# Optimization experiments

Measured on AMD Instinct MI355X. Metric: run time of the kernel, lower is better.

The kernel has to match this reference:

```python
import jax, jax.numpy as jnp
import numpy as np

B, S, D = 8, 2048, 768
NEG_SLOPE = 0.2  # PyG GATConv default LeakyReLU slope


def setup_inputs() -> dict:
    key = jax.random.key(0)
    ks = jax.random.split(key, 8)
    scale = 0.02
    return {
        "hidden_states": jax.random.normal(ks[0], (B, S, D), jnp.float32),
        "transformer_output": jax.random.normal(ks[1], (B, S, D), jnp.float32),
        "W_gat": jax.random.normal(ks[2], (D, D), jnp.float32) * scale,
        "a_src": jax.random.normal(ks[3], (D,), jnp.float32) * scale,
        "a_dst": jax.random.normal(ks[4], (D,), jnp.float32) * scale,
        "b_gat": jnp.zeros((D,), jnp.float32),
        "W_fus": jax.random.normal(ks[5], (2 * D, D), jnp.float32) * scale,
        "b_fus": jnp.zeros((D,), jnp.float32),
    }


def reference(hidden_states, transformer_output, W_gat, a_src, a_dst, b_gat, W_fus, b_fus):
    # GATConv (heads=1) over a complete graph (build_graph gives all i!=j edges,
    # PyG GATConv then adds self-loops) => dense softmax attention over all S nodes.
    xp = jnp.einsum("bsd,de->bse", hidden_states, W_gat)          # [B,S,D] transformed nodes
    alpha_src = jnp.einsum("bsd,d->bs", xp, a_src)                # score contrib of source j
    alpha_dst = jnp.einsum("bsd,d->bs", xp, a_dst)                # score contrib of target i
    # e[b,i,j] = LeakyReLU(alpha_dst[b,i] + alpha_src[b,j])
    e = jax.nn.leaky_relu(alpha_dst[:, :, None] + alpha_src[:, None, :], NEG_SLOPE)
    attn = jax.nn.softmax(e, axis=-1)                              # softmax over sources j per target i
    graph_out = jnp.einsum("bij,bjd->bid", attn, xp) + b_gat       # aggregate + bias
    fused = jnp.concatenate([transformer_output, graph_out], axis=-1)
    return jnp.einsum("bsf,fd->bsd", fused, W_fus) + b_fus
```

## Files before the change

kernel.cpp:

```cpp
#include <hip/hip_runtime.h>
#include <hip/hip_bf16.h>
#include <stdint.h>

#define B_   8
#define S_   2048
#define D_   768
#define BS_  16384
#define F_   1536

typedef __attribute__((ext_vector_type(8))) short short8;
typedef __attribute__((ext_vector_type(4))) float f32x4;
typedef __attribute__((ext_vector_type(4))) float float4v;
typedef __attribute__((ext_vector_type(4))) unsigned short ushort4v;

__device__ __forceinline__ unsigned short f2bf(float f) {
  union { float f; unsigned u; } v; v.f = f;
  unsigned r = v.u + 0x7FFFu + ((v.u >> 16) & 1u);
  return (unsigned short)(r >> 16);
}
__device__ __forceinline__ float bf2f(unsigned short h) {
  union { unsigned u; float f; } v; v.u = ((unsigned)h) << 16;
  return v.f;
}
__device__ __forceinline__ unsigned cvtpk_bf16(float lo, float hi) {
  unsigned r; asm("v_cvt_pk_bf16_f32 %0, %1, %2" : "=v"(r) : "v"(lo), "v"(hi)); return r;
}

#define GLOAD16(gp, lp) \
  __builtin_amdgcn_global_load_lds((const __attribute__((address_space(1))) void*)(gp), \
                                   (__attribute__((address_space(3))) void*)(lp), 16, 0, 0)

__global__ __launch_bounds__(256) void k_cast8(const float* __restrict__ s1,
                                               unsigned short* __restrict__ d1, int n) {
  int i = (blockIdx.x * 256 + threadIdx.x) * 8;
  if (i >= n) return;
  float4v a = *(const float4v*)(s1 + i);
  float4v b2 = *(const float4v*)(s1 + i + 4);
  union { short8 s; unsigned u[4]; } o;
  o.u[0] = cvtpk_bf16(a[0], a[1]); o.u[1] = cvtpk_bf16(a[2], a[3]);
  o.u[2] = cvtpk_bf16(b2[0], b2[1]); o.u[3] = cvtpk_bf16(b2[2], b2[3]);
  *(short8*)(d1 + i) = o.s;
}

__global__ __launch_bounds__(256) void k_transpose_cast(const float* __restrict__ src,
                                                        unsigned short* __restrict__ dst,
                                                        int R, int C) {
  __shared__ float tile[32][33];
  int bx = blockIdx.x * 32;
  int by = blockIdx.y * 32;
  int tx = threadIdx.x, ty = threadIdx.y;
#pragma unroll
  for (int k = 0; k < 32; k += 8)
    tile[ty + k][tx] = src[(size_t)(by + ty + k) * C + bx + tx];
  __syncthreads();
#pragma unroll
  for (int k = 0; k < 32; k += 8)
    dst[(size_t)(bx + ty + k) * R + by + tx] = f2bf(tile[tx][ty + k]);
}

template <int EPI>
__global__ __launch_bounds__(256, 2) void k_gemm(const unsigned short* __restrict__ A,
                                                 const unsigned short* __restrict__ A2,
                                                 const unsigned short* __restrict__ BT,
                                                 int K, int Ksplit,
                                                 float* __restrict__ outF,
                                                 const float* __restrict__ bias,
                                                 unsigned short* __restrict__ outT,
                                                 const float* __restrict__ aS,
                                                 const float* __restrict__ aD,
                                                 float* __restrict__ asO,
                                                 float* __restrict__ adO) {
  __shared__ unsigned short smem[32768];
  int lin = blockIdx.x;
  int nl  = (lin & 7) * 96 + (lin >> 3);
  int mBase = (nl / 6) * 128;
  int nBase = (nl % 6) * 128;
  int t = threadIdx.x;
  int w = t >> 6, l = t & 63;
  int lm = l & 15, lg = l >> 4;
  int wm = w >> 1, wn = w & 1;
  f32x4 acc[4][4] = {};
  const int KT = K >> 6;

  auto stage = [&](int kt, int half) {
    unsigned short* Ab = smem + half * 16384;
    unsigned short* Bb = Ab + 8192;
    const unsigned short* As = (kt < Ksplit) ? A : A2;
    int ka = (kt < Ksplit) ? kt : kt - Ksplit;
#pragma unroll
    for (int i = 0; i < 4; ++i) {
      int g = i * 256 + t;
      int r = g >> 3;
      int c = (g & 7) ^ (r & 7);
      GLOAD16(As + (size_t)(mBase + r) * 768 + ka + c * 8, (char*)Ab + i * 4096 + w * 1024);
      GLOAD16(BT + (size_t)(nBase + r) * K + kt + c * 8, (char*)Bb + i * 4096 + w * 1024);
    }
  };

  stage(0, 0);
  for (int kt = 0; kt < KT; ++kt) {
    int half = kt & 1;
    if (kt + 1 < KT) {
      stage((kt + 1) * 64, half ^ 1);
      asm volatile("s_waitcnt vmcnt(8)" ::: "memory");
    } else {
      asm volatile("s_waitcnt vmcnt(0)" ::: "memory");
    }
    __builtin_amdgcn_s_barrier();
    __builtin_amdgcn_sched_barrier(0);
    unsigned short* Ab = smem + half * 16384;
    unsigned short* Bb = Ab + 8192;
    __builtin_amdgcn_s_setprio(1);
#pragma unroll
    for (int ks = 0; ks < 2; ++ks) {
      short8 af[4], bfr[4];
#pragma unroll
      for (int mi = 0; mi < 4; ++mi) {
        int r = wm * 64 + mi * 16 + lm;
        int c = (ks * 4 + lg) ^ (r & 7);
        af[mi] = *(const short8*)(Ab + r * 64 + c * 8);
      }
#pragma unroll
      for (int ni = 0; ni < 4; ++ni) {
        int r = wn * 64 + ni * 16 + lm;
        int c = (ks * 4 + lg) ^ (r & 7);
        bfr[ni] = *(const short8*)(Bb + r * 64 + c * 8);
      }
#pragma unroll
      for (int mi = 0; mi < 4; ++mi)
#pragma unroll
        for (int ni = 0; ni < 4; ++ni)
          acc[mi][ni] = __builtin_amdgcn_mfma_f32_16x16x32_bf16(af[mi], bfr[ni], acc[mi][ni], 0, 0, 0);
    }
    __builtin_amdgcn_s_setprio(0);
    __builtin_amdgcn_sched_barrier(0);
    __builtin_amdgcn_s_barrier();
  }

  if (EPI == 0) {
#pragma unroll
    for (int mi = 0; mi < 4; ++mi) {
      int m = mBase + wm * 64 + mi * 16 + lg * 4;
#pragma unroll
      for (int ni = 0; ni < 4; ++ni) {
        int n = nBase + wn * 64 + ni * 16 + lm;
        float bv = bias[n];
#pragma unroll
        for (int r = 0; r < 4; ++r)
          outF[(size_t)(m + r) * 768 + n] = acc[mi][ni][r] + bv;
      }
    }
  } else {
#pragma unroll
    for (int mi = 0; mi < 4; ++mi) {
#pragma unroll
      for (int ni = 0; ni < 4; ++ni) {
        int col = wn * 64 + ni * 16 + lm;
#pragma unroll
        for (int r = 0; r < 4; ++r) {
          int row = wm * 64 + mi * 16 + lg * 4 + r;
          int phys = (((col >> 3) ^ (row & 7)) << 3) | (col & 7);
          smem[row * 128 + phys] = f2bf(acc[mi][ni][r]);
        }
      }
    }
    float* aLds = (float*)(smem + 16384);
    if (t < 128) {
      aLds[t] = aS[nBase + t];
      aLds[128 + t] = aD[nBase + t];
    }
    __syncthreads();
#pragma unroll
    for (int it = 0; it < 8; ++it) {
      int row = it * 16 + (t >> 4);
      int gg = t & 15;
      short8 v = *(const short8*)(&smem[row * 128 + ((gg ^ (row & 7)) << 3)]);
      *(short8*)(outT + (size_t)(mBase + row) * 768 + nBase + gg * 8) = v;
    }
    {
      int row = t >> 1, halfc = t & 1;
      float accs = 0.f, accd = 0.f;
#pragma unroll
      for (int gg = 0; gg < 8; ++gg) {
        int cq = halfc * 8 + gg;
        short8 v = *(const short8*)(&smem[row * 128 + ((cq ^ (row & 7)) << 3)]);
#pragma unroll
        for (int e = 0; e < 8; ++e) {
          float x = bf2f((unsigned short)v[e]);
          accs = fmaf(aLds[cq * 8 + e], x, accs);
          accd = fmaf(aLds[128 + cq * 8 + e], x, accd);
        }
      }
      accs += __shfl_xor(accs, 1);
      accd += __shfl_xor(accd, 1);
      if (halfc == 0) {
        atomicAdd(asO + mBase + row, accs);
        atomicAdd(adO + mBase + row, accd);
      }
    }
  }
}

__global__ __launch_bounds__(256) void k_rank(const float* __restrict__ as,
                                              float* __restrict__ ssorted, int* __restrict__ sidx,
                                              float* __restrict__ es1g, float* __restrict__ es2g,
                                              float* __restrict__ msg) {
  __shared__ float sjl[S_];
  __shared__ float red[256];
  __shared__ int rk[32][9];
  int b = blockIdx.y, t = threadIdx.x;
  float lmx = -1e30f;
#pragma unroll
  for (int q = 0; q < 2; ++q) {
    int p = (t + q * 256) * 4;
    float4v v = *(const float4v*)(as + b * S_ + p);
    *(float4v*)(sjl + p) = v;
    lmx = fmaxf(lmx, fmaxf(fmaxf(v[0], v[1]), fmaxf(v[2], v[3])));
  }
  red[t] = lmx;
  __syncthreads();
  for (int st = 128; st > 0; st >>= 1) {
    if (t < st) red[t] = fmaxf(red[t], red[t + st]);
    __syncthreads();
  }
  float Ms = red[0];
  int jl = t & 31, part = t >> 5;
  int j = blockIdx.x * 32 + jl;
  float sj = sjl[j];
  int r0 = 0, r1 = 0, r2 = 0, r3 = 0;
  int kbase = part * 256;
#pragma unroll 8
  for (int kq = 0; kq < 64; ++kq) {
    int k = kbase + kq * 4;
    float4v sk = *(const float4v*)(sjl + k);
    r0 += (sk[0] < sj) | ((sk[0] == sj) & (k < j));
    r1 += (sk[1] < sj) | ((sk[1] == sj) & (k + 1 < j));
    r2 += (sk[2] < sj) | ((sk[2] == sj) & (k + 2 < j));
    r3 += (sk[3] < sj) | ((sk[3] == sj) & (k + 3 < j));
  }
  rk[jl][part] = r0 + r1 + r2 + r3;
  __syncthreads();
  if (t < 32) {
    int rank = rk[t][0] + rk[t][1] + rk[t][2] + rk[t][3]
             + rk[t][4] + rk[t][5] + rk[t][6] + rk[t][7];
    int jj = blockIdx.x * 32 + t;
    float sv = sjl[jj];
    ssorted[b * S_ + rank] = sv;
    sidx[b * S_ + rank] = jj;
    es1g[b * S_ + rank] = __expf(sv - Ms);
    es2g[b * S_ + rank] = __expf(0.2f * (sv - Ms));
    if (blockIdx.x == 0 && t == 0) msg[b] = Ms;
  }
}

__global__ __launch_bounds__(256) void k_pscan(const float* __restrict__ es1g,
                                               const float* __restrict__ es2g,
                                               float* __restrict__ sufug,
                                               float* __restrict__ prevg) {
  __shared__ float su[256], pv[256];
  int b = blockIdx.x, t = threadIdx.x;
  float a1 = 0.f, a2 = 0.f;
#pragma unroll
  for (int r = 0; r < 8; ++r) {
    a1 += es1g[b * S_ + t * 8 + r];
    a2 += es2g[b * S_ + t * 8 + r];
  }
  su[t] = a1; pv[t] = a2;
  __syncthreads();
  for (int off = 1; off < 256; off <<= 1) {
    float vs = (t + off < 256) ? su[t + off] : 0.f;
    float vp = (t >= off) ? pv[t - off] : 0.f;
    __syncthreads();
    su[t] += vs; pv[t] += vp;
    __syncthreads();
  }
  sufug[b * 260 + t] = su[t];
  prevg[b * 260 + t] = (t > 0) ? pv[t - 1] : 0.f;
  if (t == 0) sufug[b * 260 + 256] = 0.f;
}

__global__ __launch_bounds__(192) void k_chunks(const unsigned short* __restrict__ xp,
                                                const int* __restrict__ sidx,
                                                const float* __restrict__ es1g,
                                                const float* __restrict__ es2g,
                                                float* __restrict__ SU, float* __restrict__ SV) {
  __shared__ int ridx[64];
  __shared__ float w1l[64], w2l[64];
  int b = blockIdx.y, cblk = blockIdx.x;
  int t = threadIdx.x;
  if (t < 64) {
    int r = cblk * 64 + t;
    ridx[t] = sidx[b * S_ + r];
    w1l[t] = es1g[b * S_ + r];
    w2l[t] = es2g[b * S_ + r];
  }
  __syncthreads();
  int d0 = t * 4;
  const unsigned short* xb = xp + (size_t)b * S_ * D_;
  for (int q = 0; q < 8; ++q) {
    float a1[4] = {0.f, 0.f, 0.f, 0.f}, a2[4] = {0.f, 0.f, 0.f, 0.f};
#pragma unroll
    for (int r = 0; r < 8; ++r) {
      int j = q * 8 + r;
      ushort4v xv = *(const ushort4v*)(xb + (size_t)ridx[j] * D_ + d0);
      float w1 = w1l[j], w2 = w2l[j];
#pragma unroll
      for (int e = 0; e < 4; ++e) {
        float x = bf2f(xv[e]);
        a1[e] = fmaf(w1, x, a1[e]);
        a2[e] = fmaf(w2, x, a2[e]);
      }
    }
    int c = cblk * 8 + q;
    float4v o1, o2;
    o1[0] = a1[0]; o1[1] = a1[1]; o1[2] = a1[2]; o1[3] = a1[3];
    o2[0] = a2[0]; o2[1] = a2[1]; o2[2] = a2[2]; o2[3] = a2[3];
    *(float4v*)(SU + ((size_t)b * 257 + c) * D_ + d0) = o1;
    *(float4v*)(SV + ((size_t)b * 256 + c) * D_ + d0) = o2;
  }
}

__global__ __launch_bounds__(256) void k_scan(float* __restrict__ SU, float* __restrict__ SV) {
  __shared__ float sums[8][33];
  int b = blockIdx.y;
  int dl = threadIdx.x & 31, p = threadIdx.x >> 5;
  int d = blockIdx.x * 32 + dl;
  float* u = SU + (size_t)b * 257 * D_ + d;
  float* v = SV + (size_t)b * 256 * D_ + d;
  int c0 = p * 32;
  float cu[32], cv[32];
  float su_ = 0.f, sv_ = 0.f;
#pragma unroll
  for (int q = 0; q < 32; ++q) {
    cu[q] = u[(size_t)(c0 + q) * D_];
    cv[q] = v[(size_t)(c0 + q) * D_];
    su_ += cu[q]; sv_ += cv[q];
  }
  sums[p][dl] = su_;
  __syncthreads();
  float offU = 0.f;
#pragma unroll
  for (int q = 0; q < 8; ++q) if (q > p) offU += sums[q][dl];
  __syncthreads();
  sums[p][dl] = sv_;
  __syncthreads();
  float offV = 0.f;
#pragma unroll
  for (int q = 0; q < 8; ++q) if (q < p) offV += sums[q][dl];
  float run = offU;
#pragma unroll
  for (int q = 31; q >= 0; --q) { run += cu[q]; u[(size_t)(c0 + q) * D_] = run; }
  float pr = offV;
#pragma unroll
  for (int q = 0; q < 32; ++q) { v[(size_t)(c0 + q) * D_] = pr; pr += cv[q]; }
  if (p == 0) u[(size_t)256 * D_] = 0.f;
}

__global__ __launch_bounds__(256) void k_out(const unsigned short* __restrict__ xp,
                                             const float* __restrict__ ad,
                                             const float* __restrict__ ssorted,
                                             const int* __restrict__ sidx,
                                             const float* __restrict__ es1g,
                                             const float* __restrict__ es2g,
                                             const float* __restrict__ sufug,
                                             const float* __restrict__ prevg,
                                             const float* __restrict__ msg,
                                             const float* __restrict__ SU,
                                             const float* __restrict__ SV,
                                             const float* __restrict__ b_gat,
                                             const float* __restrict__ to,
                                             unsigned short* __restrict__ to_bf,
                                             unsigned short* __restrict__ gout) {
  __shared__ float skeys[2048];
  __shared__ float G1[8], G2[8], WL[8][8];
  __shared__ int CI[8], RI[8][8];
  int bid = blockIdx.x;
  int b = bid & 7, itile = bid >> 3;
  int i0 = itile * 8;
  int t = threadIdx.x;
#pragma unroll
  for (int k2 = 0; k2 < 2; ++k2) {
    int p = (t + k2 * 256) * 4;
    *(float4v*)(skeys + p) = *(const float4v*)(ssorted + b * S_ + p);
  }
  __syncthreads();
  if (t < 8) {
    int i = i0 + t;
    float di = ad[b * S_ + i];
    float thr = -di;
    int lo = 0, hi = 2048;
#pragma unroll
    for (int st = 0; st < 11; ++st) {
      int mid = (lo + hi) >> 1;
      if (skeys[mid] <= thr) lo = mid + 1; else hi = mid;
    }
    int c = lo >> 3; if (c > 255) c = 255;
    float t1 = di + msg[b];
    float mst = fmaxf(t1, 0.2f * t1);
    float g1 = __expf(t1 - mst), g2 = __expf(0.2f * t1 - mst);
    float den = g1 * sufug[b * 260 + c + 1] + g2 * prevg[b * 260 + c];
    float wr[8]; int rid[8];
#pragma unroll
    for (int r = 0; r < 8; ++r) {
      int row = c * 8 + r;
      bool neg = (skeys[row] <= thr);
      float wv = neg ? g2 * es2g[b * S_ + row] : g1 * es1g[b * S_ + row];
      den += wv;
      wr[r] = wv;
      rid[r] = sidx[b * S_ + row];
    }
    float inv = 1.f / den;
    G1[t] = g1 * inv; G2[t] = g2 * inv; CI[t] = c;
#pragma unroll
    for (int r = 0; r < 8; ++r) { WL[t][r] = wr[r] * inv; RI[t][r] = rid[r]; }
  }
  __syncthreads();
  int w = t >> 6, lane = t & 63;
  int dbase = lane * 4;
  float4v bgv[3];
#pragma unroll
  for (int q = 0; q < 3; ++q) bgv[q] = *(const float4v*)(b_gat + dbase + q * 256);
  const unsigned short* xb = xp + (size_t)b * S_ * D_;
  const float* SUb = SU + (size_t)b * 257 * D_;
  const float* SVb = SV + (size_t)b * 256 * D_;
#pragma unroll
  for (int rep = 0; rep < 2; ++rep) {
    int ii = w + rep * 4;
    int c = CI[ii];
    float g1 = G1[ii], g2 = G2[ii];
    size_t roff = ((size_t)(b * S_ + i0 + ii)) * D_;
    float4v o[3];
#pragma unroll
    for (int q = 0; q < 3; ++q) {
      int d = dbase + q * 256;
      float4v uu = *(const float4v*)(SUb + (size_t)(c + 1) * D_ + d);
      float4v vv = *(const float4v*)(SVb + (size_t)c * D_ + d);
#pragma unroll
      for (int e = 0; e < 4; ++e) o[q][e] = fmaf(g1, uu[e], g2 * vv[e]);
    }
#pragma unroll
    for (int q = 0; q < 3; ++q) {
      int d = dbase + q * 256;
      float4v tv = *(const float4v*)(to + roff + d);
      ushort4v ow;
      ow[0] = f2bf(tv[0]); ow[1] = f2bf(tv[1]); ow[2] = f2bf(tv[2]); ow[3] = f2bf(tv[3]);
      *(ushort4v*)(to_bf + roff + d) = ow;
    }
#pragma unroll
    for (int r = 0; r < 8; ++r) {
      float wv = WL[ii][r];
      const unsigned short* xr = xb + (size_t)RI[ii][r] * D_;
#pragma unroll
      for (int q = 0; q < 3; ++q) {
        int d = dbase + q * 256;
        ushort4v xv = *(const ushort4v*)(xr + d);
#pragma unroll
        for (int e = 0; e < 4; ++e) o[q][e] = fmaf(wv, bf2f(xv[e]), o[q][e]);
      }
    }
#pragma unroll
    for (int q = 0; q < 3; ++q) {
      int d = dbase + q * 256;
      ushort4v og;
      og[0] = f2bf(o[q][0] + bgv[q][0]); og[1] = f2bf(o[q][1] + bgv[q][1]);
      og[2] = f2bf(o[q][2] + bgv[q][2]); og[3] = f2bf(o[q][3] + bgv[q][3]);
      *(ushort4v*)(gout + roff + d) = og;
    }
  }
}

extern "C" void kernel_launch(void* const* d_in, const int* in_sizes, int n_in,
                              void* d_out, int out_size, void* d_ws, size_t ws_size,
                              hipStream_t stream) {
  const float* hs   = (const float*)d_in[0];
  const float* to   = (const float*)d_in[1];
  const float* Wg   = (const float*)d_in[2];
  const float* asrc = (const float*)d_in[3];
  const float* adst = (const float*)d_in[4];
  const float* bg   = (const float*)d_in[5];
  const float* Wf   = (const float*)d_in[6];
  const float* bfu  = (const float*)d_in[7];
  float* out = (float*)d_out;

  char* ws = (char*)d_ws;
  size_t off = 0;
  auto alloc = [&](size_t bytes) {
    char* p = ws + off;
    off += (bytes + 255) & ~(size_t)255;
    return p;
  };
  unsigned short* hs_bf = (unsigned short*)alloc((size_t)BS_ * D_ * 2);
  unsigned short* to_bf = (unsigned short*)alloc((size_t)BS_ * D_ * 2);
  unsigned short* xp    = (unsigned short*)alloc((size_t)BS_ * D_ * 2);
  unsigned short* WgT   = (unsigned short*)alloc((size_t)D_ * D_ * 2);
  unsigned short* WfT   = (unsigned short*)alloc((size_t)D_ * F_ * 2);
  float* as   = (float*)alloc((size_t)BS_ * 4);
  float* ad   = (float*)alloc((size_t)BS_ * 4);
  float* ssorted = (float*)alloc((size_t)BS_ * 4);
  int*   sidx    = (int*)alloc((size_t)BS_ * 4);
  float* es1g = (float*)alloc((size_t)BS_ * 4);
  float* es2g = (float*)alloc((size_t)BS_ * 4);
  float* sufug = (float*)alloc((size_t)B_ * 260 * 4);
  float* prevg = (float*)alloc((size_t)B_ * 260 * 4);
  float* msg   = (float*)alloc(256);
  float* SU = (float*)alloc((size_t)B_ * 257 * D_ * 4);
  float* SV = (float*)alloc((size_t)B_ * 256 * D_ * 4);
  unsigned short* gout = hs_bf;

  int n = BS_ * D_;
  hipMemsetAsync(as, 0, (size_t)BS_ * 4, stream);
  hipMemsetAsync(ad, 0, (size_t)BS_ * 4, stream);
  k_cast8<<<n / 2048, 256, 0, stream>>>(hs, hs_bf, n);
  k_transpose_cast<<<dim3(D_ / 32, D_ / 32), dim3(32, 8), 0, stream>>>(Wg, WgT, D_, D_);
  k_transpose_cast<<<dim3(D_ / 32, F_ / 32), dim3(32, 8), 0, stream>>>(Wf, WfT, F_, D_);
  k_gemm<1><<<768, 256, 0, stream>>>(hs_bf, hs_bf, WgT, D_, D_, nullptr, nullptr, xp,
                                     asrc, adst, as, ad);
  k_rank<<<dim3(64, B_), 256, 0, stream>>>(as, ssorted, sidx, es1g, es2g, msg);
  k_pscan<<<B_, 256, 0, stream>>>(es1g, es2g, sufug, prevg);
  k_chunks<<<dim3(32, B_), 192, 0, stream>>>(xp, sidx, es1g, es2g, SU, SV);
  k_scan<<<dim3(24, B_), 256, 0, stream>>>(SU, SV);
  k_out<<<2048, 256, 0, stream>>>(xp, ad, ssorted, sidx, es1g, es2g, sufug, prevg, msg,
                                  SU, SV, bg, to, to_bf, gout);
  k_gemm<0><<<768, 256, 0, stream>>>(to_bf, gout, WfT, F_, D_, out, bfu, nullptr,
                                     nullptr, nullptr, nullptr, nullptr);
}
```

Measured before the change: 157.9 us.

## Halve GEMM K-tile to raise occupancy and move transformer-output cast into cast kernel

New measurement: 165.1 us. 1.05x slower.

```diff
diff --git a/kernel.cpp b/kernel.cpp
--- a/kernel.cpp
+++ b/kernel.cpp
@@ -30,16 +30,28 @@
   __builtin_amdgcn_global_load_lds((const __attribute__((address_space(1))) void*)(gp), \
                                    (__attribute__((address_space(3))) void*)(lp), 16, 0, 0)
 
-__global__ __launch_bounds__(256) void k_cast8(const float* __restrict__ s1,
-                                               unsigned short* __restrict__ d1, int n) {
+__global__ __launch_bounds__(256) void k_cast8x2(const float* __restrict__ s1,
+                                                 const float* __restrict__ s2,
+                                                 unsigned short* __restrict__ d1,
+                                                 unsigned short* __restrict__ d2, int n) {
   int i = (blockIdx.x * 256 + threadIdx.x) * 8;
   if (i >= n) return;
-  float4v a = *(const float4v*)(s1 + i);
-  float4v b2 = *(const float4v*)(s1 + i + 4);
-  union { short8 s; unsigned u[4]; } o;
-  o.u[0] = cvtpk_bf16(a[0], a[1]); o.u[1] = cvtpk_bf16(a[2], a[3]);
-  o.u[2] = cvtpk_bf16(b2[0], b2[1]); o.u[3] = cvtpk_bf16(b2[2], b2[3]);
-  *(short8*)(d1 + i) = o.s;
+  {
+    float4v a = *(const float4v*)(s1 + i);
+    float4v b2 = *(const float4v*)(s1 + i + 4);
+    union { short8 s; unsigned u[4]; } o;
+    o.u[0] = cvtpk_bf16(a[0], a[1]); o.u[1] = cvtpk_bf16(a[2], a[3]);
+    o.u[2] = cvtpk_bf16(b2[0], b2[1]); o.u[3] = cvtpk_bf16(b2[2], b2[3]);
+    *(short8*)(d1 + i) = o.s;
+  }
+  {
+    float4v a = *(const float4v*)(s2 + i);
+    float4v b2 = *(const float4v*)(s2 + i + 4);
+    union { short8 s; unsigned u[4]; } o;
+    o.u[0] = cvtpk_bf16(a[0], a[1]); o.u[1] = cvtpk_bf16(a[2], a[3]);
+    o.u[2] = cvtpk_bf16(b2[0], b2[1]); o.u[3] = cvtpk_bf16(b2[2], b2[3]);
+    *(short8*)(d2 + i) = o.s;
+  }
 }
 
 __global__ __launch_bounds__(256) void k_transpose_cast(const float* __restrict__ src,
@@ -59,7 +71,7 @@
 }
 
 template <int EPI>
-__global__ __launch_bounds__(256, 2) void k_gemm(const unsigned short* __restrict__ A,
+__global__ __launch_bounds__(256, 4) void k_gemm(const unsigned short* __restrict__ A,
                                                  const unsigned short* __restrict__ A2,
                                                  const unsigned short* __restrict__ BT,
                                                  int K, int Ksplit,
@@ -70,7 +82,7 @@
                                                  const float* __restrict__ aD,
                                                  float* __restrict__ asO,
                                                  float* __restrict__ adO) {
-  __shared__ unsigned short smem[32768];
+  __shared__ unsigned short smem[16896];
   int lin = blockIdx.x;
   int nl  = (lin & 7) * 96 + (lin >> 3);
   int mBase = (nl / 6) * 128;
@@ -80,58 +92,58 @@
   int lm = l & 15, lg = l >> 4;
   int wm = w >> 1, wn = w & 1;
   f32x4 acc[4][4] = {};
-  const int KT = K >> 6;
-
-  auto stage = [&](int kt, int half) {
-    unsigned short* Ab = smem + half * 16384;
-    unsigned short* Bb = Ab + 8192;
+  const int NS = K >> 5;
+
+  auto stage = [&](int j, int h) {
+    unsigned short* Ab = smem + h * 8192;
+    unsigned short* Bb = Ab + 4096;
+    int kt = j * 32;
     const unsigned short* As = (kt < Ksplit) ? A : A2;
     int ka = (kt < Ksplit) ? kt : kt - Ksplit;
 #pragma unroll
-    for (int i = 0; i < 4; ++i) {
+    for (int i = 0; i < 2; ++i) {
       int g = i * 256 + t;
-      int r = g >> 3;
-      int c = (g & 7) ^ (r & 7);
+      int r = g >> 2, c = (g & 3) ^ (r & 3);
       GLOAD16(As + (size_t)(mBase + r) * 768 + ka + c * 8, (char*)Ab + i * 4096 + w * 1024);
+    }
+#pragma unroll
+    for (int i = 0; i < 2; ++i) {
+      int g = i * 256 + t;
+      int r = g >> 2, c = (g & 3) ^ (r & 3);
       GLOAD16(BT + (size_t)(nBase + r) * K + kt + c * 8, (char*)Bb + i * 4096 + w * 1024);
     }
   };
 
   stage(0, 0);
-  for (int kt = 0; kt < KT; ++kt) {
-    int half = kt & 1;
-    if (kt + 1 < KT) {
-      stage((kt + 1) * 64, half ^ 1);
-      asm volatile("s_waitcnt vmcnt(8)" ::: "memory");
+  for (int j = 0; j < NS; ++j) {
+    int h = j & 1;
+    if (j + 1 < NS) {
+      stage(j + 1, h ^ 1);
+      asm volatile("s_waitcnt vmcnt(4)" ::: "memory");
     } else {
       asm volatile("s_waitcnt vmcnt(0)" ::: "memory");
     }
     __builtin_amdgcn_s_barrier();
     __builtin_amdgcn_sched_barrier(0);
-    unsigned short* Ab = smem + half * 16384;
-    unsigned short* Bb = Ab + 8192;
+    unsigned short* Ab = smem + h * 8192;
+    unsigned short* Bb = Ab + 4096;
+    short8 af[4], bfr[4];
+#pragma unroll
+    for (int mi = 0; mi < 4; ++mi) {
+      int r = wm * 64 + mi * 16 + lm;
+      af[mi] = *(const short8*)(Ab + r * 32 + (lg ^ (r & 3)) * 8);
+    }
+#pragma unroll
+    for (int ni = 0; ni < 4; ++ni) {
+      int r = wn * 64 + ni * 16 + lm;
+      bfr[ni] = *(const short8*)(Bb + r * 32 + (lg ^ (r & 3)) * 8);
+    }
     __builtin_amdgcn_s_setprio(1);
 #pragma unroll
-    for (int ks = 0; ks < 2; ++ks) {
-      short8 af[4], bfr[4];
-#pragma unroll
-      for (int mi = 0; mi < 4; ++mi) {
-        int r = wm * 64 + mi * 16 + lm;
-        int c = (ks * 4 + lg) ^ (r & 7);
-        af[mi] = *(const short8*)(Ab + r * 64 + c * 8);
-      }
-#pragma unroll
-      for (int ni = 0; ni < 4; ++ni) {
-        int r = wn * 64 + ni * 16 + lm;
-        int c = (ks * 4 + lg) ^ (r & 7);
-        bfr[ni] = *(const short8*)(Bb + r * 64 + c * 8);
-      }
-#pragma unroll
-      for (int mi = 0; mi < 4; ++mi)
-#pragma unroll
-        for (int ni = 0; ni < 4; ++ni)
-          acc[mi][ni] = __builtin_amdgcn_mfma_f32_16x16x32_bf16(af[mi], bfr[ni], acc[mi][ni], 0, 0, 0);
-    }
+    for (int mi = 0; mi < 4; ++mi)
+#pragma unroll
+      for (int ni = 0; ni < 4; ++ni)
+        acc[mi][ni] = __builtin_amdgcn_mfma_f32_16x16x32_bf16(af[mi], bfr[ni], acc[mi][ni], 0, 0, 0);
     __builtin_amdgcn_s_setprio(0);
     __builtin_amdgcn_sched_barrier(0);
     __builtin_amdgcn_s_barrier();
@@ -151,6 +163,7 @@
       }
     }
   } else {
+    __syncthreads();
 #pragma unroll
     for (int mi = 0; mi < 4; ++mi) {
 #pragma unroll
@@ -368,8 +381,6 @@
                                              const float* __restrict__ SU,
                                              const float* __restrict__ SV,
                                              const float* __restrict__ b_gat,
-                                             const float* __restrict__ to,
-                                             unsigned short* __restrict__ to_bf,
                                              unsigned short* __restrict__ gout) {
   __shared__ float skeys[2048];
   __shared__ float G1[8], G2[8], WL[8][8];
@@ -437,14 +448,6 @@
       float4v vv = *(const float4v*)(SVb + (size_t)c * D_ + d);
 #pragma unroll
       for (int e = 0; e < 4; ++e) o[q][e] = fmaf(g1, uu[e], g2 * vv[e]);
-    }
-#pragma unroll
-    for (int q = 0; q < 3; ++q) {
-      int d = dbase + q * 256;
-      float4v tv = *(const float4v*)(to + roff + d);
-      ushort4v ow;
-      ow[0] = f2bf(tv[0]); ow[1] = f2bf(tv[1]); ow[2] = f2bf(tv[2]); ow[3] = f2bf(tv[3]);
-      *(ushort4v*)(to_bf + roff + d) = ow;
     }
 #pragma unroll
     for (int r = 0; r < 8; ++r) {
@@ -510,7 +513,7 @@
   int n = BS_ * D_;
   hipMemsetAsync(as, 0, (size_t)BS_ * 4, stream);
   hipMemsetAsync(ad, 0, (size_t)BS_ * 4, stream);
-  k_cast8<<<n / 2048, 256, 0, stream>>>(hs, hs_bf, n);
+  k_cast8x2<<<n / 2048, 256, 0, stream>>>(hs, to, hs_bf, to_bf, n);
   k_transpose_cast<<<dim3(D_ / 32, D_ / 32), dim3(32, 8), 0, stream>>>(Wg, WgT, D_, D_);
   k_transpose_cast<<<dim3(D_ / 32, F_ / 32), dim3(32, 8), 0, stream>>>(Wf, WfT, F_, D_);
   k_gemm<1><<<768, 256, 0, stream>>>(hs_bf, hs_bf, WgT, D_, D_, nullptr, nullptr, xp,
@@ -520,7 +523,7 @@
   k_chunks<<<dim3(32, B_), 192, 0, stream>>>(xp, sidx, es1g, es2g, SU, SV);
   k_scan<<<dim3(24, B_), 256, 0, stream>>>(SU, SV);
   k_out<<<2048, 256, 0, stream>>>(xp, ad, ssorted, sidx, es1g, es2g, sufug, prevg, msg,
-                                  SU, SV, bg, to, to_bf, gout);
+                                  SU, SV, bg, gout);
   k_gemm<0><<<768, 256, 0, stream>>>(to_bf, gout, WfT, F_, D_, out, bfu, nullptr,
                                      nullptr, nullptr, nullptr, nullptr);
 }
```
